# Kernel optimization log

Hardware: AMD Instinct MI355X
Metric: run time of the kernel (lower is better)

Reference implementation:

```python
import jax, jax.numpy as jnp
import numpy as np
import math

MAX_LEN = 5000

def _build_pe(d_feat: int, dtype=jnp.float32) -> jnp.ndarray:
    # d_model rounded up to even, as in run_once
    d_model = int(math.ceil(d_feat / 2) * 2)
    pos = jnp.arange(MAX_LEN, dtype=dtype)[:, None]                       # [L,1]
    div = jnp.exp(jnp.arange(0, d_model, 2, dtype=dtype)
                  * (-math.log(10000.0) / d_model))                       # [d_model/2]
    pe = jnp.zeros((MAX_LEN, d_model), dtype=dtype)
    pe = pe.at[:, 0::2].set(jnp.sin(pos * div))
    pe = pe.at[:, 1::2].set(jnp.cos(pos * div))
    return pe

def setup_inputs() -> dict:
    key = jax.random.key(0)
    k1, k2 = jax.random.split(key)
    B, S, D = 32, 4096, 256
    nodes = jax.random.normal(k1, (B, S, D), dtype=jnp.float32)
    num_nodes = jax.random.randint(k2, (B,), 0, S, dtype=jnp.int64 if jax.config.read('jax_enable_x64') else jnp.int32)
    return {"nodes": nodes, "num_nodes": num_nodes}

def reference(nodes, num_nodes):
    # torch: pe.roll(center,0)[i] = pe[(i-center) % MAX_LEN]; add to nodes[b,:center+1]
    B, S, D = nodes.shape
    pe = _build_pe(D, nodes.dtype)                                        # [L, d_model]
    i = jnp.arange(S)                                                     # [S]
    idx = (i[None, :] - num_nodes[:, None]) % MAX_LEN                     # [B,S]
    mask = i[None, :] <= num_nodes[:, None]                               # [B,S]
    add = pe[idx, :D]                                                     # [B,S,D] gather
    return nodes + jnp.where(mask[:, :, None], add, jnp.zeros((), nodes.dtype))
```

## Files before the change

kernel.cpp:

```cpp
#include <hip/hip_runtime.h>
#include <math.h>


typedef float v4f __attribute__((ext_vector_type(4)));

#define BLOCK 256
#define BATCH 4

template <bool EXACT>
__global__ __launch_bounds__(BLOCK) void rpe_kernel(const float* __restrict__ nodes,
                                                    const int* __restrict__ num_nodes,
                                                    float* __restrict__ out,
                                                    const int total4) {
    const int stride = gridDim.x * BLOCK;
    const int tid    = blockIdx.x * BLOCK + threadIdx.x;

    const int d4 = tid & 63;
    const float cexp   = -0.051905126482062035f;
    const float inv2pi = 0.15915494309189535f;
    const float f0 = exp2f(cexp * (float)(4 * d4)) * inv2pi;
    const float f1 = exp2f(cexp * (float)(4 * d4 + 2)) * inv2pi;

    for (int base = tid; base < total4; base += stride * BATCH) {
        int idx[BATCH];
        v4f v[BATCH];
        int nn[BATCH];

        #pragma unroll
        for (int k = 0; k < BATCH; ++k) {
            idx[k] = base + k * stride;
            if (EXACT || idx[k] < total4) {
                v[k] = reinterpret_cast<const v4f*>(nodes)[idx[k]];
                const int b = __builtin_amdgcn_readfirstlane(idx[k] >> 18);
                nn[k] = num_nodes[b];
            }
        }

        #pragma unroll
        for (int k = 0; k < BATCH; ++k) {
            if (!EXACT && idx[k] >= total4) break;
            const int s = (idx[k] >> 6) & 4095;
            v4f w = v[k];
            if (s <= nn[k]) {
                int r = s - nn[k];
                int p = (r < 0) ? r + 5000 : r;
                const float pf = (float)p;

                float r0 = pf * f0;  r0 -= floorf(r0);
                float r1 = pf * f1;  r1 -= floorf(r1);

                w.x += __builtin_amdgcn_sinf(r0);
                w.y += __builtin_amdgcn_cosf(r0);
                w.z += __builtin_amdgcn_sinf(r1);
                w.w += __builtin_amdgcn_cosf(r1);
            }
            __builtin_nontemporal_store(w, reinterpret_cast<v4f*>(out) + idx[k]);
        }
    }
}

extern "C" void kernel_launch(void* const* d_in, const int* in_sizes, int n_in,
                              void* d_out, int out_size, void* d_ws, size_t ws_size,
                              hipStream_t stream) {
    const float* nodes     = (const float*)d_in[0];
    const int*   num_nodes = (const int*)d_in[1];
    float*       out       = (float*)d_out;

    const int total4 = out_size / 4;

    int grid = (total4 + BLOCK * BATCH - 1) / (BLOCK * BATCH);
    if (grid > 2048) grid = 2048;

    const long long chunk = (long long)grid * BLOCK * BATCH;
    if (total4 % chunk == 0) {
        rpe_kernel<true><<<grid, BLOCK, 0, stream>>>(nodes, num_nodes, out, total4);
    } else {
        rpe_kernel<false><<<grid, BLOCK, 0, stream>>>(nodes, num_nodes, out, total4);
    }
}
```

Baseline: 238.8 us.

## Replace grid-stride batched loop with one-element-per-thread kernel and nontemporal loads

After: 219.5 us. -8.1%, faster.

```diff
diff --git a/kernel.cpp b/kernel.cpp
--- a/kernel.cpp
+++ b/kernel.cpp
@@ -4,59 +4,41 @@
 
 typedef float v4f __attribute__((ext_vector_type(4)));
 
-#define BLOCK 256
-#define BATCH 4
-
-template <bool EXACT>
-__global__ __launch_bounds__(BLOCK) void rpe_kernel(const float* __restrict__ nodes,
-                                                    const int* __restrict__ num_nodes,
-                                                    float* __restrict__ out,
-                                                    const int total4) {
-    const int stride = gridDim.x * BLOCK;
-    const int tid    = blockIdx.x * BLOCK + threadIdx.x;
+__global__ __launch_bounds__(256) void rpe_kernel(const float* __restrict__ nodes,
+                                                  const int* __restrict__ num_nodes,
+                                                  float* __restrict__ out,
+                                                  const int total4) {
+    const int tid = blockIdx.x * blockDim.x + threadIdx.x;
+    if (tid >= total4) return;
 
     const int d4 = tid & 63;
-    const float cexp   = -0.051905126482062035f;
-    const float inv2pi = 0.15915494309189535f;
-    const float f0 = exp2f(cexp * (float)(4 * d4)) * inv2pi;
-    const float f1 = exp2f(cexp * (float)(4 * d4 + 2)) * inv2pi;
+    const int s  = (tid >> 6) & 4095;
+    const int b  = tid >> 18;
 
-    for (int base = tid; base < total4; base += stride * BATCH) {
-        int idx[BATCH];
-        v4f v[BATCH];
-        int nn[BATCH];
+    const int nn = num_nodes[b];
 
-        #pragma unroll
-        for (int k = 0; k < BATCH; ++k) {
-            idx[k] = base + k * stride;
-            if (EXACT || idx[k] < total4) {
-                v[k] = reinterpret_cast<const v4f*>(nodes)[idx[k]];
-                const int b = __builtin_amdgcn_readfirstlane(idx[k] >> 18);
-                nn[k] = num_nodes[b];
-            }
-        }
+    v4f v = __builtin_nontemporal_load(reinterpret_cast<const v4f*>(nodes) + tid);
 
-        #pragma unroll
-        for (int k = 0; k < BATCH; ++k) {
-            if (!EXACT && idx[k] >= total4) break;
-            const int s = (idx[k] >> 6) & 4095;
-            v4f w = v[k];
-            if (s <= nn[k]) {
-                int r = s - nn[k];
-                int p = (r < 0) ? r + 5000 : r;
-                const float pf = (float)p;
+    if (s <= nn) {
+        int r = s - nn;
+        int p = (r < 0) ? r + 5000 : r;
+        const float pf = (float)p;
 
-                float r0 = pf * f0;  r0 -= floorf(r0);
-                float r1 = pf * f1;  r1 -= floorf(r1);
+        const float cexp   = -0.051905126482062035f;
+        const float inv2pi = 0.15915494309189535f;
+        const float f0 = exp2f(cexp * (float)(4 * d4)) * inv2pi;
+        const float f1 = exp2f(cexp * (float)(4 * d4 + 2)) * inv2pi;
 
-                w.x += __builtin_amdgcn_sinf(r0);
-                w.y += __builtin_amdgcn_cosf(r0);
-                w.z += __builtin_amdgcn_sinf(r1);
-                w.w += __builtin_amdgcn_cosf(r1);
-            }
-            __builtin_nontemporal_store(w, reinterpret_cast<v4f*>(out) + idx[k]);
-        }
+        float r0 = pf * f0;  r0 -= floorf(r0);
+        float r1 = pf * f1;  r1 -= floorf(r1);
+
+        v.x += __builtin_amdgcn_sinf(r0);
+        v.y += __builtin_amdgcn_cosf(r0);
+        v.z += __builtin_amdgcn_sinf(r1);
+        v.w += __builtin_amdgcn_cosf(r1);
     }
+
+    __builtin_nontemporal_store(v, reinterpret_cast<v4f*>(out) + tid);
 }
 
 extern "C" void kernel_launch(void* const* d_in, const int* in_sizes, int n_in,
@@ -67,14 +49,8 @@
     float*       out       = (float*)d_out;
 
     const int total4 = out_size / 4;
+    const int block  = 256;
+    const int grid   = (total4 + block - 1) / block;
 
-    int grid = (total4 + BLOCK * BATCH - 1) / (BLOCK * BATCH);
-    if (grid > 2048) grid = 2048;
-
-    const long long chunk = (long long)grid * BLOCK * BATCH;
-    if (total4 % chunk == 0) {
-        rpe_kernel<true><<<grid, BLOCK, 0, stream>>>(nodes, num_nodes, out, total4);
-    } else {
-        rpe_kernel<false><<<grid, BLOCK, 0, stream>>>(nodes, num_nodes, out, total4);
-    }
+    rpe_kernel<<<grid, block, 0, stream>>>(nodes, num_nodes, out, total4);
 }
```
